# Optimization experiments

Measured on AMD Instinct MI355X. Metric: run time of the kernel, lower is better.

Reference implementation:

```python
import jax, jax.numpy as jnp
import numpy as np

T, H, E, K, I = 2048, 2048, 64, 8, 768
CAP = 512


def setup_inputs() -> dict:
    key = jax.random.key(0)
    ks = jax.random.split(key, 5)
    s = 0.02
    return {
        "hidden_states": jax.random.normal(ks[0], (T, H), jnp.float32),
        "w_router": jax.random.normal(ks[1], (E, H), jnp.float32) * s,
        "w_gate": jax.random.normal(ks[2], (E, H, I), jnp.float32) * s,
        "w_up": jax.random.normal(ks[3], (E, H, I), jnp.float32) * s,
        "w_down": jax.random.normal(ks[4], (E, I, H), jnp.float32) * s,
    }


def _moe(x, w_router, w_gate, w_up, w_down):
    Tn = x.shape[0]
    # --- router: softmax -> top-k -> renormalize (norm_topk_prob=True) ---
    logits = x @ w_router.T                                   # [T, E]
    probs = jax.nn.softmax(logits.astype(jnp.float32), axis=-1)
    topk_w, topk_idx = jax.lax.top_k(probs, K)                # [T, K]
    topk_w = topk_w / jnp.sum(topk_w, axis=-1, keepdims=True)
    # --- dispatch: sort (token, expert) pairs by expert, scatter into capacity buffers ---
    e = topk_idx.reshape(-1)                                  # [T*K] expert id per pair
    t = jnp.repeat(jnp.arange(Tn), K)                         # [T*K] token id per pair
    w = topk_w.reshape(-1)                                    # [T*K] combine weight per pair
    order = jnp.argsort(e, stable=True)
    e_s, t_s, w_s = e[order], t[order], w[order]
    counts = jax.ops.segment_sum(jnp.ones_like(e_s), e_s, num_segments=E)  # [E]
    starts = jnp.cumsum(counts) - counts                      # start offset of each expert group
    pos = jnp.arange(Tn * K) - starts[e_s]                    # slot within expert
    valid = pos < CAP
    posc = jnp.where(valid, pos, 0)
    vm = valid.astype(x.dtype)[:, None]
    buf = jnp.zeros((E, CAP, H), x.dtype).at[e_s, posc].add(x[t_s] * vm)   # [E, C, H]
    # --- grouped expert SwiGLU FFN: down(silu(gate(x)) * up(x)) ---
    g = jnp.einsum('ech,ehi->eci', buf, w_gate)               # [E, C, I]
    u = jnp.einsum('ech,ehi->eci', buf, w_up)                 # [E, C, I]
    y = jnp.einsum('eci,eih->ech', jax.nn.silu(g) * u, w_down)  # [E, C, H]
    # --- combine: gather expert outputs back to tokens, weighted sum ---
    gw = (w_s.astype(x.dtype) * valid.astype(x.dtype))[:, None]
    out = jnp.zeros((Tn, H), x.dtype).at[t_s].add(gw * y[e_s, posc])
    return out


def reference(hidden_states, w_router, w_gate, w_up, w_down):
    return _moe(hidden_states, w_router, w_gate, w_up, w_down)
```

## Files before the change

### kernel.cpp

```cpp
#include <hip/hip_runtime.h>
#include <hip/hip_bf16.h>
#include <math.h>

#define T_TOK 2048
#define H_DIM 2048
#define NEXP  64
#define TOPK  8
#define I_DIM 768
#define CAPE  512
#define MTMAX 4
#define LDW   40

typedef short bf16x8 __attribute__((ext_vector_type(8)));
typedef float f32x4  __attribute__((ext_vector_type(4)));

__device__ __forceinline__ unsigned short f2bf(float f) {
  unsigned u = __float_as_uint(f);
  u += 0x7fffu + ((u >> 16) & 1u);
  return (unsigned short)(u >> 16);
}
__device__ __forceinline__ float bf2f(unsigned short b) {
  return __uint_as_float(((unsigned)b) << 16);
}
__device__ __forceinline__ unsigned pack2(float lo, float hi) {
  __hip_bfloat162 h = __float22bfloat162_rn(make_float2(lo, hi));
  unsigned r; __builtin_memcpy(&r, &h, 4); return r;
}

__global__ __launch_bounds__(256) void k_xcvt(const float* __restrict__ x,
                                              unsigned short* __restrict__ xb) {
  const size_t i = ((size_t)blockIdx.x * 256 + threadIdx.x) * 8;
  float4 p = *(const float4*)(x + i);
  float4 q = *(const float4*)(x + i + 4);
  union { unsigned u[4]; bf16x8 v; } r;
  r.u[0] = pack2(p.x, p.y); r.u[1] = pack2(p.z, p.w);
  r.u[2] = pack2(q.x, q.y); r.u[3] = pack2(q.z, q.w);
  *(bf16x8*)(xb + i) = r.v;
}

__global__ __launch_bounds__(256) void k_router(const float* __restrict__ x,
                                                const float* __restrict__ wr,
                                                int* __restrict__ topk_idx,
                                                float* __restrict__ topk_w) {
  const int lane = threadIdx.x & 63;
  const int t = blockIdx.x * 4 + (threadIdx.x >> 6);
  const float4* xr   = (const float4*)(x + (size_t)t * H_DIM);
  const float4* wrow = (const float4*)(wr + (size_t)lane * H_DIM);
  double acc = 0.0;
  for (int i = 0; i < H_DIM / 4; ++i) {
    float4 a = xr[i], b = wrow[i];
    acc += (double)a.x * b.x; acc += (double)a.y * b.y;
    acc += (double)a.z * b.z; acc += (double)a.w * b.w;
  }
  float cur = (float)acc;
  float val[TOPK]; int idx[TOPK];
#pragma unroll
  for (int r = 0; r < TOPK; ++r) {
    float bv = cur; int bi = lane;
#pragma unroll
    for (int off = 32; off > 0; off >>= 1) {
      float ov = __shfl_xor(bv, off);
      int   oi = __shfl_xor(bi, off);
      if (ov > bv || (ov == bv && oi < bi)) { bv = ov; bi = oi; }
    }
    val[r] = bv; idx[r] = bi;
    if (lane == bi) cur = -INFINITY;
  }
  float m = val[0], s = 0.f, w[TOPK];
#pragma unroll
  for (int r = 0; r < TOPK; ++r) { w[r] = expf(val[r] - m); s += w[r]; }
  if (lane < TOPK) {
    topk_idx[t * TOPK + lane] = idx[lane];
    topk_w [t * TOPK + lane] = w[lane] / s;
  }
}

__global__ __launch_bounds__(1024) void k_rank(const int* __restrict__ topk_idx,
                                               int* __restrict__ pair_pos,
                                               int* __restrict__ slot_token,
                                               int* __restrict__ cnts) {
  __shared__ int s_run[64];
  __shared__ int s_whist[16][64];
  const int tid = threadIdx.x, lane = tid & 63, wv = tid >> 6;
  const int sub = wv >> 2;
  if (tid < 64) s_run[tid] = 0;
  for (int it = 0; it < 16; ++it) {
    const int p = (it * 4 + sub) * 256 + (tid & 255);
    const int e = topk_idx[p];
    __syncthreads();
    s_whist[wv][lane] = 0;
    __syncthreads();
    unsigned long long m = ~0ull;
#pragma unroll
    for (int b = 0; b < 6; ++b) {
      unsigned long long bb = __ballot((e >> b) & 1);
      m &= ((e >> b) & 1) ? bb : ~bb;
    }
    const int rw = __popcll(m & ((1ull << lane) - 1ull));
    if (rw == 0) s_whist[wv][e] = __popcll(m);
    __syncthreads();
    int off = rw;
    for (int w2 = 0; w2 < wv; ++w2) off += s_whist[w2][e];
    const int pos = s_run[e] + off;
    pair_pos[p] = pos;
    if (pos < CAPE) slot_token[e * CAPE + pos] = p >> 3;
    __syncthreads();
    if (tid < 64) {
      int tsum = 0;
#pragma unroll
      for (int w2 = 0; w2 < 16; ++w2) tsum += s_whist[w2][tid];
      s_run[tid] += tsum;
    }
  }
  __syncthreads();
  if (tid < 64) cnts[tid] = s_run[tid];
}

__global__ __launch_bounds__(512) void k_gateup(const unsigned short* __restrict__ xb,
                                                const float* __restrict__ wg,
                                                const float* __restrict__ wu,
                                                const int* __restrict__ slot_token,
                                                const int* __restrict__ cnts,
                                                unsigned short* __restrict__ act) {
  const int NB = NEXP * MTMAX * 6;
  const int v = (blockIdx.x & 7) * (NB / 8) + (blockIdx.x >> 3);
  const int e = v / (MTMAX * 6);
  const int rem = v % (MTMAX * 6);
  const int mt = rem / 6, nt = rem % 6;

  int cnt = cnts[e]; cnt = cnt < CAPE ? cnt : CAPE;
  if (cnt <= 0 || mt * 128 >= cnt) return;
  const int m0 = mt << 7;

  __shared__ __align__(16) short As[2][128 * LDW];
  __shared__ __align__(16) short Bg[2][128 * LDW];
  __shared__ __align__(16) short Bu[2][128 * LDW];

  const int tid = threadIdx.x;
  const int lane = tid & 63, wave = tid >> 6;
  const int wm = wave >> 2, wn = wave & 3;
  const int lr = lane & 15, lg = lane >> 4;

  const int a_row = tid >> 2, a_ko = (tid & 3) * 8;
  const int b_mat = tid >> 8;
  const int b_idx = tid & 255;
  const int b_kq = b_idx & 7, b_nq = b_idx >> 3;
  const size_t wbase = (size_t)e * H_DIM * I_DIM + (size_t)nt * 128;

  const int tok = (m0 + a_row < cnt) ? slot_token[e * CAPE + m0 + a_row] : 0;
  const unsigned short* xr = xb + (size_t)tok * H_DIM + a_ko;
  const float* bp  = (b_mat ? wu : wg) + wbase + (size_t)(4 * b_kq) * I_DIM + 4 * b_nq;
  short* Bdst0 = b_mat ? Bu[0] : Bg[0];
  short* Bdst1 = b_mat ? Bu[1] : Bg[1];

  f32x4 accg[4][2], accu[4][2];
#pragma unroll
  for (int mi = 0; mi < 4; ++mi)
#pragma unroll
    for (int ni = 0; ni < 2; ++ni) {
      accg[mi][ni] = (f32x4){0.f, 0.f, 0.f, 0.f};
      accu[mi][ni] = (f32x4){0.f, 0.f, 0.f, 0.f};
    }

  struct Tile { bf16x8 a; float4 b[4]; };

  auto LOAD = [&](Tile& Tl, int kt) {
    const int k0 = kt * 32;
    Tl.a = *(const bf16x8*)(xr + k0);
    const float* r0 = bp + (size_t)k0 * I_DIM;
#pragma unroll
    for (int j = 0; j < 4; ++j)
      Tl.b[j] = *(const float4*)(r0 + (size_t)j * I_DIM);
  };
  auto STORE = [&](const Tile& Tl, int b) {
    *(bf16x8*)(&As[b][a_row * LDW + a_ko]) = Tl.a;
    short* Bd = b ? Bdst1 : Bdst0;
    const float* q0 = (const float*)&Tl.b[0];
    const float* q1 = (const float*)&Tl.b[1];
    const float* q2 = (const float*)&Tl.b[2];
    const float* q3 = (const float*)&Tl.b[3];
#pragma unroll
    for (int i = 0; i < 4; ++i) {
      uint2 w = { pack2(q0[i], q1[i]), pack2(q2[i], q3[i]) };
      *(uint2*)(&Bd[(4 * b_nq + i) * LDW + 4 * b_kq]) = w;
    }
  };
  auto COMPUTE = [&](int b) {
    bf16x8 a[4], bg[2], bu[2];
#pragma unroll
    for (int mi = 0; mi < 4; ++mi)
      a[mi] = *(const bf16x8*)(&As[b][(wm * 64 + mi * 16 + lr) * LDW + lg * 8]);
#pragma unroll
    for (int ni = 0; ni < 2; ++ni) {
      bg[ni] = *(const bf16x8*)(&Bg[b][(wn * 32 + ni * 16 + lr) * LDW + lg * 8]);
      bu[ni] = *(const bf16x8*)(&Bu[b][(wn * 32 + ni * 16 + lr) * LDW + lg * 8]);
    }
#pragma unroll
    for (int mi = 0; mi < 4; ++mi)
#pragma unroll
      for (int ni = 0; ni < 2; ++ni) {
        accg[mi][ni] = __builtin_amdgcn_mfma_f32_16x16x32_bf16(a[mi], bg[ni], accg[mi][ni], 0, 0, 0);
        accu[mi][ni] = __builtin_amdgcn_mfma_f32_16x16x32_bf16(a[mi], bu[ni], accu[mi][ni], 0, 0, 0);
      }
  };

  const int NK = H_DIM / 32;
  Tile tA, tB;
  LOAD(tA, 0);
  STORE(tA, 0);
  LOAD(tB, 1);
  __syncthreads();

  int t = 0;
#pragma unroll 1
  for (; t + 2 < NK; t += 2) {
    LOAD(tA, t + 2);
    COMPUTE(0);
    STORE(tB, 1);
    __syncthreads();
    LOAD(tB, t + 3);
    COMPUTE(1);
    STORE(tA, 0);
    __syncthreads();
  }
  COMPUTE(0);
  STORE(tB, 1);
  __syncthreads();
  COMPUTE(1);

#pragma unroll
  for (int mi = 0; mi < 4; ++mi)
#pragma unroll
    for (int ni = 0; ni < 2; ++ni)
#pragma unroll
      for (int r = 0; r < 4; ++r) {
        const int row = m0 + wm * 64 + mi * 16 + lg * 4 + r;
        const int col = nt * 128 + wn * 32 + ni * 16 + lr;
        const float g = accg[mi][ni][r], u = accu[mi][ni][r];
        const float vv = (g / (1.f + __expf(-g))) * u;
        act[(size_t)(e * CAPE + row) * I_DIM + col] = f2bf(vv);
      }
}

__global__ __launch_bounds__(512) void k_down(const unsigned short* __restrict__ act,
                                              const float* __restrict__ wd,
                                              const int* __restrict__ cnts,
                                              unsigned short* __restrict__ y) {
  const int NB = NEXP * MTMAX * 16;
  const int v = (blockIdx.x & 7) * (NB / 8) + (blockIdx.x >> 3);
  const int e = v / (MTMAX * 16);
  const int rem = v % (MTMAX * 16);
  const int mt = rem / 16, nt = rem % 16;

  int cnt = cnts[e]; cnt = cnt < CAPE ? cnt : CAPE;
  if (cnt <= 0 || mt * 128 >= cnt) return;
  const int m0 = mt << 7;

  __shared__ __align__(16) short As[2][128 * LDW];
  __shared__ __align__(16) short Bt[2][128 * LDW];

  const int tid = threadIdx.x;
  const int lane = tid & 63, wave = tid >> 6;
  const int wm = wave >> 2, wn = wave & 3;
  const int lr = lane & 15, lg = lane >> 4;

  const int role = tid >> 8;
  const int ridx = tid & 255;
  const int b_kq = ridx & 7, b_nq = ridx >> 3;
  const int a_row = ridx >> 1, a_half = ridx & 1;
  const size_t wbase = (size_t)e * I_DIM * H_DIM + (size_t)nt * 128;

  const unsigned short* ap = act + (size_t)(e * CAPE + m0 + a_row) * I_DIM + a_half * 16;
  const float* bp = wd + wbase + (size_t)(4 * b_kq) * H_DIM + 4 * b_nq;

  f32x4 acc[4][2];
#pragma unroll
  for (int mi = 0; mi < 4; ++mi)
#pragma unroll
    for (int ni = 0; ni < 2; ++ni) acc[mi][ni] = (f32x4){0.f, 0.f, 0.f, 0.f};

  struct Tile { bf16x8 a0, a1; float4 b[4]; };

  auto LOAD = [&](Tile& Tl, int kt) {
    const int k0 = kt * 32;
    if (role) {
      Tl.a0 = *(const bf16x8*)(ap + k0);
      Tl.a1 = *(const bf16x8*)(ap + k0 + 8);
    } else {
      const float* r0 = bp + (size_t)k0 * H_DIM;
#pragma unroll
      for (int j = 0; j < 4; ++j)
        Tl.b[j] = *(const float4*)(r0 + (size_t)j * H_DIM);
    }
  };
  auto STORE = [&](const Tile& Tl, int b) {
    if (role) {
      *(bf16x8*)(&As[b][a_row * LDW + a_half * 16])     = Tl.a0;
      *(bf16x8*)(&As[b][a_row * LDW + a_half * 16 + 8]) = Tl.a1;
    } else {
      const float* q0 = (const float*)&Tl.b[0];
      const float* q1 = (const float*)&Tl.b[1];
      const float* q2 = (const float*)&Tl.b[2];
      const float* q3 = (const float*)&Tl.b[3];
#pragma unroll
      for (int i = 0; i < 4; ++i) {
        uint2 w = { pack2(q0[i], q1[i]), pack2(q2[i], q3[i]) };
        *(uint2*)(&Bt[b][(4 * b_nq + i) * LDW + 4 * b_kq]) = w;
      }
    }
  };
  auto COMPUTE = [&](int b) {
    bf16x8 a[4], bb[2];
#pragma unroll
    for (int mi = 0; mi < 4; ++mi)
      a[mi] = *(const bf16x8*)(&As[b][(wm * 64 + mi * 16 + lr) * LDW + lg * 8]);
#pragma unroll
    for (int ni = 0; ni < 2; ++ni)
      bb[ni] = *(const bf16x8*)(&Bt[b][(wn * 32 + ni * 16 + lr) * LDW + lg * 8]);
#pragma unroll
    for (int mi = 0; mi < 4; ++mi)
#pragma unroll
      for (int ni = 0; ni < 2; ++ni)
        acc[mi][ni] = __builtin_amdgcn_mfma_f32_16x16x32_bf16(a[mi], bb[ni], acc[mi][ni], 0, 0, 0);
  };

  const int NK = I_DIM / 32;
  Tile tA, tB;
  LOAD(tA, 0);
  STORE(tA, 0);
  LOAD(tB, 1);
  __syncthreads();

  int t = 0;
#pragma unroll 1
  for (; t + 2 < NK; t += 2) {
    LOAD(tA, t + 2);
    COMPUTE(0);
    STORE(tB, 1);
    __syncthreads();
    LOAD(tB, t + 3);
    COMPUTE(1);
    STORE(tA, 0);
    __syncthreads();
  }
  COMPUTE(0);
  STORE(tB, 1);
  __syncthreads();
  COMPUTE(1);

#pragma unroll
  for (int mi = 0; mi < 4; ++mi)
#pragma unroll
    for (int ni = 0; ni < 2; ++ni)
#pragma unroll
      for (int r = 0; r < 4; ++r) {
        const int row = m0 + wm * 64 + mi * 16 + lg * 4 + r;
        const int col = nt * 128 + wn * 32 + ni * 16 + lr;
        y[(size_t)(e * CAPE + row) * H_DIM + col] = f2bf(acc[mi][ni][r]);
      }
}

__global__ __launch_bounds__(256) void k_combine(const unsigned short* __restrict__ y,
                                                 const int* __restrict__ topk_idx,
                                                 const float* __restrict__ topk_w,
                                                 const int* __restrict__ pair_pos,
                                                 float* __restrict__ out) {
  const int t = blockIdx.x;
  __shared__ int s_e[TOPK]; __shared__ int s_p[TOPK]; __shared__ float s_w[TOPK];
  if (threadIdx.x < TOPK) {
    s_e[threadIdx.x] = topk_idx[t * TOPK + threadIdx.x];
    s_p[threadIdx.x] = pair_pos[t * TOPK + threadIdx.x];
    s_w[threadIdx.x] = topk_w [t * TOPK + threadIdx.x];
  }
  __syncthreads();
  const int h0 = threadIdx.x * 8;
  float acc[8] = {0.f, 0.f, 0.f, 0.f, 0.f, 0.f, 0.f, 0.f};
#pragma unroll
  for (int k = 0; k < TOPK; ++k) {
    const int pos = s_p[k];
    if (pos >= CAPE) continue;
    const float w = s_w[k];
    const bf16x8 vv = *(const bf16x8*)(&y[(size_t)(s_e[k] * CAPE + pos) * H_DIM + h0]);
#pragma unroll
    for (int j = 0; j < 8; ++j) acc[j] += w * bf2f((unsigned short)vv[j]);
  }
  float4 o0 = {acc[0], acc[1], acc[2], acc[3]};
  float4 o1 = {acc[4], acc[5], acc[6], acc[7]};
  *(float4*)(out + (size_t)t * H_DIM + h0)     = o0;
  *(float4*)(out + (size_t)t * H_DIM + h0 + 4) = o1;
}

extern "C" void kernel_launch(void* const* d_in, const int* in_sizes, int n_in,
                              void* d_out, int out_size, void* d_ws, size_t ws_size,
                              hipStream_t stream) {
  const float* x   = (const float*)d_in[0];
  const float* wr  = (const float*)d_in[1];
  const float* wgt = (const float*)d_in[2];
  const float* wup = (const float*)d_in[3];
  const float* wdn = (const float*)d_in[4];
  float* out = (float*)d_out;

  char* ws = (char*)d_ws;
  int*            topk_idx   = (int*)(ws);
  float*          topk_w     = (float*)(ws + 65536);
  int*            pair_pos   = (int*)(ws + 131072);
  int*            cnts       = (int*)(ws + 196608);
  int*            slot_token = (int*)(ws + 196864);
  unsigned short* xb         = (unsigned short*)(ws + 327936);
  unsigned short* act        = (unsigned short*)(ws + 327936 + 8388608);
  unsigned short* yb         = (unsigned short*)(ws + 327936 + 8388608 + 50331648);

  k_xcvt   <<<dim3(T_TOK * H_DIM / 2048), dim3(256), 0, stream>>>(x, xb);
  k_router <<<dim3(T_TOK / 4),        dim3(256), 0, stream>>>(x, wr, topk_idx, topk_w);
  k_rank   <<<dim3(1),                dim3(1024), 0, stream>>>(topk_idx, pair_pos, slot_token, cnts);
  k_gateup <<<dim3(NEXP * MTMAX * 6), dim3(512), 0, stream>>>(xb, wgt, wup, slot_token, cnts, act);
  k_down   <<<dim3(NEXP * MTMAX * 16),dim3(512), 0, stream>>>(act, wdn, cnts, yb);
  k_combine<<<dim3(T_TOK),            dim3(256), 0, stream>>>(yb, topk_idx, topk_w, pair_pos, out);
}
```

Before: 735.6 us.

## Stage activation tiles via async global-to-LDS loads with four-deep A buffering

Replaces register-staged A-tile loads in the gate/up and down expert GEMMs with direct global-to-LDS async loads (global_load_lds, 16 bytes per lane). A now uses a 4-slot unpadded LDS ring while the fp32 weight tiles keep their register-convert double buffer, and the main loop is unrolled by four. The aim is to cut VGPR pressure and the LDS store instructions for A, and to let A prefetch run further ahead. It also switches the router dot product from double to float FMA and adds an occupancy hint to k_down. The unpadded A layout may cause LDS bank conflicts, and the change relies on barriers to cover async-load completion.

```diff
diff --git a/kernel.cpp b/kernel.cpp
--- a/kernel.cpp
+++ b/kernel.cpp
@@ -25,6 +25,11 @@
 __device__ __forceinline__ unsigned pack2(float lo, float hi) {
   __hip_bfloat162 h = __float22bfloat162_rn(make_float2(lo, hi));
   unsigned r; __builtin_memcpy(&r, &h, 4); return r;
+}
+__device__ __forceinline__ void async16(void* lds, const unsigned short* g) {
+  __builtin_amdgcn_global_load_lds(
+      (const __attribute__((address_space(1))) unsigned int*)(const void*)g,
+      (__attribute__((address_space(3))) unsigned int*)lds, 16, 0, 0);
 }
 
 __global__ __launch_bounds__(256) void k_xcvt(const float* __restrict__ x,
@@ -46,13 +51,13 @@
   const int t = blockIdx.x * 4 + (threadIdx.x >> 6);
   const float4* xr   = (const float4*)(x + (size_t)t * H_DIM);
   const float4* wrow = (const float4*)(wr + (size_t)lane * H_DIM);
-  double acc = 0.0;
+  float acc = 0.f;
   for (int i = 0; i < H_DIM / 4; ++i) {
     float4 a = xr[i], b = wrow[i];
-    acc += (double)a.x * b.x; acc += (double)a.y * b.y;
-    acc += (double)a.z * b.z; acc += (double)a.w * b.w;
-  }
-  float cur = (float)acc;
+    acc = fmaf(a.x, b.x, acc); acc = fmaf(a.y, b.y, acc);
+    acc = fmaf(a.z, b.z, acc); acc = fmaf(a.w, b.w, acc);
+  }
+  float cur = acc;
   float val[TOPK]; int idx[TOPK];
 #pragma unroll
   for (int r = 0; r < TOPK; ++r) {
@@ -132,7 +137,7 @@
   if (cnt <= 0 || mt * 128 >= cnt) return;
   const int m0 = mt << 7;
 
-  __shared__ __align__(16) short As[2][128 * LDW];
+  __shared__ __align__(16) short Asl[4][128 * 32];
   __shared__ __align__(16) short Bg[2][128 * LDW];
   __shared__ __align__(16) short Bu[2][128 * LDW];
 
@@ -141,14 +146,14 @@
   const int wm = wave >> 2, wn = wave & 3;
   const int lr = lane & 15, lg = lane >> 4;
 
-  const int a_row = tid >> 2, a_ko = (tid & 3) * 8;
+  const int arow = wave * 16 + (lane >> 2);
+  const int tokA = (m0 + arow < cnt) ? slot_token[e * CAPE + m0 + arow] : 0;
+  const unsigned short* axg = xb + (size_t)tokA * H_DIM + (lane & 3) * 8;
+
   const int b_mat = tid >> 8;
   const int b_idx = tid & 255;
   const int b_kq = b_idx & 7, b_nq = b_idx >> 3;
   const size_t wbase = (size_t)e * H_DIM * I_DIM + (size_t)nt * 128;
-
-  const int tok = (m0 + a_row < cnt) ? slot_token[e * CAPE + m0 + a_row] : 0;
-  const unsigned short* xr = xb + (size_t)tok * H_DIM + a_ko;
   const float* bp  = (b_mat ? wu : wg) + wbase + (size_t)(4 * b_kq) * I_DIM + 4 * b_nq;
   short* Bdst0 = b_mat ? Bu[0] : Bg[0];
   short* Bdst1 = b_mat ? Bu[1] : Bg[1];
@@ -162,18 +167,18 @@
       accu[mi][ni] = (f32x4){0.f, 0.f, 0.f, 0.f};
     }
 
-  struct Tile { bf16x8 a; float4 b[4]; };
-
-  auto LOAD = [&](Tile& Tl, int kt) {
-    const int k0 = kt * 32;
-    Tl.a = *(const bf16x8*)(xr + k0);
-    const float* r0 = bp + (size_t)k0 * I_DIM;
+  struct Tile { float4 b[4]; };
+
+  auto ALOAD = [&](int j, int kt) {
+    async16(&Asl[j][wave * 512], axg + (size_t)kt * 32);
+  };
+  auto LOADB = [&](Tile& Tl, int kt) {
+    const float* r0 = bp + (size_t)(kt * 32) * I_DIM;
 #pragma unroll
     for (int j = 0; j < 4; ++j)
       Tl.b[j] = *(const float4*)(r0 + (size_t)j * I_DIM);
   };
-  auto STORE = [&](const Tile& Tl, int b) {
-    *(bf16x8*)(&As[b][a_row * LDW + a_ko]) = Tl.a;
+  auto STOREB = [&](const Tile& Tl, int b) {
     short* Bd = b ? Bdst1 : Bdst0;
     const float* q0 = (const float*)&Tl.b[0];
     const float* q1 = (const float*)&Tl.b[1];
@@ -185,15 +190,15 @@
       *(uint2*)(&Bd[(4 * b_nq + i) * LDW + 4 * b_kq]) = w;
     }
   };
-  auto COMPUTE = [&](int b) {
+  auto COMPUTE = [&](int ja, int jb) {
     bf16x8 a[4], bg[2], bu[2];
 #pragma unroll
     for (int mi = 0; mi < 4; ++mi)
-      a[mi] = *(const bf16x8*)(&As[b][(wm * 64 + mi * 16 + lr) * LDW + lg * 8]);
+      a[mi] = *(const bf16x8*)(&Asl[ja][(wm * 64 + mi * 16 + lr) * 32 + lg * 8]);
 #pragma unroll
     for (int ni = 0; ni < 2; ++ni) {
-      bg[ni] = *(const bf16x8*)(&Bg[b][(wn * 32 + ni * 16 + lr) * LDW + lg * 8]);
-      bu[ni] = *(const bf16x8*)(&Bu[b][(wn * 32 + ni * 16 + lr) * LDW + lg * 8]);
+      bg[ni] = *(const bf16x8*)(&Bg[jb][(wn * 32 + ni * 16 + lr) * LDW + lg * 8]);
+      bu[ni] = *(const bf16x8*)(&Bu[jb][(wn * 32 + ni * 16 + lr) * LDW + lg * 8]);
     }
 #pragma unroll
     for (int mi = 0; mi < 4; ++mi)
@@ -206,27 +211,28 @@
 
   const int NK = H_DIM / 32;
   Tile tA, tB;
-  LOAD(tA, 0);
-  STORE(tA, 0);
-  LOAD(tB, 1);
+  ALOAD(0, 0); ALOAD(1, 1);
+  LOADB(tA, 0); STOREB(tA, 0);
+  LOADB(tB, 1);
   __syncthreads();
 
-  int t = 0;
 #pragma unroll 1
-  for (; t + 2 < NK; t += 2) {
-    LOAD(tA, t + 2);
-    COMPUTE(0);
-    STORE(tB, 1);
-    __syncthreads();
-    LOAD(tB, t + 3);
-    COMPUTE(1);
-    STORE(tA, 0);
-    __syncthreads();
-  }
-  COMPUTE(0);
-  STORE(tB, 1);
-  __syncthreads();
-  COMPUTE(1);
+  for (int t = 0; t + 7 < NK; t += 4) {
+    ALOAD(2, t + 2); LOADB(tA, t + 2);
+    COMPUTE(0, 0); STOREB(tB, 1); __syncthreads();
+    ALOAD(3, t + 3); LOADB(tB, t + 3);
+    COMPUTE(1, 1); STOREB(tA, 0); __syncthreads();
+    ALOAD(0, t + 4); LOADB(tA, t + 4);
+    COMPUTE(2, 0); STOREB(tB, 1); __syncthreads();
+    ALOAD(1, t + 5); LOADB(tB, t + 5);
+    COMPUTE(3, 1); STOREB(tA, 0); __syncthreads();
+  }
+  ALOAD(2, NK - 2); LOADB(tA, NK - 2);
+  COMPUTE(0, 0); STOREB(tB, 1); __syncthreads();
+  ALOAD(3, NK - 1); LOADB(tB, NK - 1);
+  COMPUTE(1, 1); STOREB(tA, 0); __syncthreads();
+  COMPUTE(2, 0); STOREB(tB, 1); __syncthreads();
+  COMPUTE(3, 1);
 
 #pragma unroll
   for (int mi = 0; mi < 4; ++mi)
@@ -242,10 +248,10 @@
       }
 }
 
-__global__ __launch_bounds__(512) void k_down(const unsigned short* __restrict__ act,
-                                              const float* __restrict__ wd,
-                                              const int* __restrict__ cnts,
-                                              unsigned short* __restrict__ y) {
+__global__ __launch_bounds__(512, 6) void k_down(const unsigned short* __restrict__ act,
+                                                 const float* __restrict__ wd,
+                                                 const int* __restrict__ cnts,
+                                                 unsigned short* __restrict__ y) {
   const int NB = NEXP * MTMAX * 16;
   const int v = (blockIdx.x & 7) * (NB / 8) + (blockIdx.x >> 3);
   const int e = v / (MTMAX * 16);
@@ -256,7 +262,7 @@
   if (cnt <= 0 || mt * 128 >= cnt) return;
   const int m0 = mt << 7;
 
-  __shared__ __align__(16) short As[2][128 * LDW];
+  __shared__ __align__(16) short Asl[4][128 * 32];
   __shared__ __align__(16) short Bt[2][128 * LDW];
 
   const int tid = threadIdx.x;
@@ -264,13 +270,12 @@
   const int wm = wave >> 2, wn = wave & 3;
   const int lr = lane & 15, lg = lane >> 4;
 
-  const int role = tid >> 8;
-  const int ridx = tid & 255;
-  const int b_kq = ridx & 7, b_nq = ridx >> 3;
-  const int a_row = ridx >> 1, a_half = ridx & 1;
+  const int arow = wave * 16 + (lane >> 2);
+  const unsigned short* apg = act + (size_t)(e * CAPE + m0 + arow) * I_DIM + (lane & 3) * 8;
+
+  const int b_kq = tid & 7, b_nq = (tid >> 3) & 31;
+  const bool bstage = (tid < 256);
   const size_t wbase = (size_t)e * I_DIM * H_DIM + (size_t)nt * 128;
-
-  const unsigned short* ap = act + (size_t)(e * CAPE + m0 + a_row) * I_DIM + a_half * 16;
   const float* bp = wd + wbase + (size_t)(4 * b_kq) * H_DIM + 4 * b_nq;
 
   f32x4 acc[4][2];
@@ -279,44 +284,38 @@
 #pragma unroll
     for (int ni = 0; ni < 2; ++ni) acc[mi][ni] = (f32x4){0.f, 0.f, 0.f, 0.f};
 
-  struct Tile { bf16x8 a0, a1; float4 b[4]; };
-
-  auto LOAD = [&](Tile& Tl, int kt) {
-    const int k0 = kt * 32;
-    if (role) {
-      Tl.a0 = *(const bf16x8*)(ap + k0);
-      Tl.a1 = *(const bf16x8*)(ap + k0 + 8);
-    } else {
-      const float* r0 = bp + (size_t)k0 * H_DIM;
-#pragma unroll
-      for (int j = 0; j < 4; ++j)
-        Tl.b[j] = *(const float4*)(r0 + (size_t)j * H_DIM);
-    }
-  };
-  auto STORE = [&](const Tile& Tl, int b) {
-    if (role) {
-      *(bf16x8*)(&As[b][a_row * LDW + a_half * 16])     = Tl.a0;
-      *(bf16x8*)(&As[b][a_row * LDW + a_half * 16 + 8]) = Tl.a1;
-    } else {
-      const float* q0 = (const float*)&Tl.b[0];
-      const float* q1 = (const float*)&Tl.b[1];
-      const float* q2 = (const float*)&Tl.b[2];
-      const float* q3 = (const float*)&Tl.b[3];
-#pragma unroll
-      for (int i = 0; i < 4; ++i) {
-        uint2 w = { pack2(q0[i], q1[i]), pack2(q2[i], q3[i]) };
-        *(uint2*)(&Bt[b][(4 * b_nq + i) * LDW + 4 * b_kq]) = w;
-      }
-    }
-  };
-  auto COMPUTE = [&](int b) {
+  struct Tile { float4 b[4]; };
+
+  auto ALOAD = [&](int j, int kt) {
+    async16(&Asl[j][wave * 512], apg + (size_t)kt * 32);
+  };
+  auto LOADB = [&](Tile& Tl, int kt) {
+    if (!bstage) return;
+    const float* r0 = bp + (size_t)(kt * 32) * H_DIM;
+#pragma unroll
+    for (int j = 0; j < 4; ++j)
+      Tl.b[j] = *(const float4*)(r0 + (size_t)j * H_DIM);
+  };
+  auto STOREB = [&](const Tile& Tl, int b) {
+    if (!bstage) return;
+    const float* q0 = (const float*)&Tl.b[0];
+    const float* q1 = (const float*)&Tl.b[1];
+    const float* q2 = (const float*)&Tl.b[2];
+    const float* q3 = (const float*)&Tl.b[3];
+#pragma unroll
+    for (int i = 0; i < 4; ++i) {
+      uint2 w = { pack2(q0[i], q1[i]), pack2(q2[i], q3[i]) };
+      *(uint2*)(&Bt[b][(4 * b_nq + i) * LDW + 4 * b_kq]) = w;
+    }
+  };
+  auto COMPUTE = [&](int ja, int jb) {
     bf16x8 a[4], bb[2];
 #pragma unroll
     for (int mi = 0; mi < 4; ++mi)
-      a[mi] = *(const bf16x8*)(&As[b][(wm * 64 + mi * 16 + lr) * LDW + lg * 8]);
+      a[mi] = *(const bf16x8*)(&Asl[ja][(wm * 64 + mi * 16 + lr) * 32 + lg * 8]);
 #pragma unroll
     for (int ni = 0; ni < 2; ++ni)
-      bb[ni] = *(const bf16x8*)(&Bt[b][(wn * 32 + ni * 16 + lr) * LDW + lg * 8]);
+      bb[ni] = *(const bf16x8*)(&Bt[jb][(wn * 32 + ni * 16 + lr) * LDW + lg * 8]);
 #pragma unroll
     for (int mi = 0; mi < 4; ++mi)
 #pragma unroll
@@ -326,27 +325,28 @@
 
   const int NK = I_DIM / 32;
   Tile tA, tB;
-  LOAD(tA, 0);
-  STORE(tA, 0);
-  LOAD(tB, 1);
+  ALOAD(0, 0); ALOAD(1, 1);
+  LOADB(tA, 0); STOREB(tA, 0);
+  LOADB(tB, 1);
   __syncthreads();
 
-  int t = 0;
 #pragma unroll 1
-  for (; t + 2 < NK; t += 2) {
-    LOAD(tA, t + 2);
-    COMPUTE(0);
-    STORE(tB, 1);
-    __syncthreads();
-    LOAD(tB, t + 3);
-    COMPUTE(1);
-    STORE(tA, 0);
-    __syncthreads();
-  }
-  COMPUTE(0);
-  STORE(tB, 1);
-  __syncthreads();
-  COMPUTE(1);
+  for (int t = 0; t + 7 < NK; t += 4) {
+    ALOAD(2, t + 2); LOADB(tA, t + 2);
+    COMPUTE(0, 0); STOREB(tB, 1); __syncthreads();
+    ALOAD(3, t + 3); LOADB(tB, t + 3);
+    COMPUTE(1, 1); STOREB(tA, 0); __syncthreads();
+    ALOAD(0, t + 4); LOADB(tA, t + 4);
+    COMPUTE(2, 0); STOREB(tB, 1); __syncthreads();
+    ALOAD(1, t + 5); LOADB(tB, t + 5);
+    COMPUTE(3, 1); STOREB(tA, 0); __syncthreads();
+  }
+  ALOAD(2, NK - 2); LOADB(tA, NK - 2);
+  COMPUTE(0, 0); STOREB(tB, 1); __syncthreads();
+  ALOAD(3, NK - 1); LOADB(tB, NK - 1);
+  COMPUTE(1, 1); STOREB(tA, 0); __syncthreads();
+  COMPUTE(2, 0); STOREB(tB, 1); __syncthreads();
+  COMPUTE(3, 1);
 
 #pragma unroll
   for (int mi = 0; mi < 4; ++mi)
```

New measurement: 1.017 ms. 1.38x slower.
